# Optimization experiments

Hardware: AMD Instinct MI355X
Metric: run time of the kernel (lower is better)

The kernel has to match this reference:

```python
import jax, jax.numpy as jnp
import numpy as np

N_HEAD = 16
MASK_NEG = 1e10  # matches torch's -10000000000.0 * (1 - b)


def setup_inputs() -> dict:
    key = jax.random.key(0)
    ks = jax.random.split(key, 9)
    B, S, D = 2, 2048, 2048
    std = 0.02
    inp = {
        "x": jax.random.normal(ks[0], (B, S, D), dtype=jnp.float32),
        "Wq": jax.random.normal(ks[1], (D, D), dtype=jnp.float32) * std,
        "bq": jnp.zeros((D,), dtype=jnp.float32),
        "Wk": jax.random.normal(ks[2], (D, D), dtype=jnp.float32) * std,
        "bk": jnp.zeros((D,), dtype=jnp.float32),
        "Wv": jax.random.normal(ks[3], (D, D), dtype=jnp.float32) * std,
        "bv": jnp.zeros((D,), dtype=jnp.float32),
        "Wd": jax.random.normal(ks[4], (D, D), dtype=jnp.float32) * std,
        "bd": jnp.zeros((D,), dtype=jnp.float32),
    }
    return inp


def reference(x, Wq, bq, Wk, bk, Wv, bv, Wd, bd):
    # x: [B, S, D]; layer_past=None, query=None path (full causal prefill)
    B, S, D = x.shape
    H = N_HEAD
    hd = D // H

    def split(h):  # [B,S,D] -> [B,H,S,hd]
        return h.reshape(B, S, H, hd).transpose(0, 2, 1, 3)

    q = split(x @ Wq + bq)
    k = split(x @ Wk + bk)
    v = split(x @ Wv + bv)

    # scores [B,H,S,S]; scale=True divides by sqrt(head_dim)
    w = jnp.einsum("bhqd,bhkd->bhqk", q, k) / jnp.sqrt(jnp.float32(hd))
    b = jnp.tril(jnp.ones((S, S), dtype=w.dtype))  # causal bias buffer slice
    w = w * b - MASK_NEG * (1.0 - b)
    w = jax.nn.softmax(w, axis=-1)
    a = jnp.einsum("bhqk,bhkd->bhqd", w, v)

    a = a.transpose(0, 2, 1, 3).reshape(B, S, D)  # merge_heads
    a = a @ Wd + bd
    present = jnp.stack((k, v))  # [2, B, H, S, hd]
    return a, present
```

## Files before the change

kernel.cpp:

```cpp
#include <hip/hip_runtime.h>


typedef unsigned short ushort_t;
typedef __attribute__((ext_vector_type(8))) short short8;
typedef __attribute__((ext_vector_type(4))) float f32x4;

#define MFMA16x16x32 __builtin_amdgcn_mfma_f32_16x16x32_bf16
#define S_LEN   2048
#define DMODEL  2048
#define A_ELEMS 8388608
#define W_ELEMS 4194304

__device__ __forceinline__ ushort_t f2bf(float x) {
  unsigned u = __float_as_uint(x);
  u += 0x7FFFu + ((u >> 16) & 1u);
  return (ushort_t)(u >> 16);
}
__device__ __forceinline__ unsigned pack2(float lo, float hi) {
  return (unsigned)f2bf(lo) | ((unsigned)f2bf(hi) << 16);
}
struct f8 { float v[8]; };
__device__ __forceinline__ f8 ld8f(const float* p) {
  f8 r;
  float4 a = *(const float4*)p, b = *(const float4*)(p + 4);
  r.v[0]=a.x; r.v[1]=a.y; r.v[2]=a.z; r.v[3]=a.w;
  r.v[4]=b.x; r.v[5]=b.y; r.v[6]=b.z; r.v[7]=b.w;
  return r;
}
__device__ __forceinline__ uint4 cvt8(const f8& f) {
  uint4 o;
  o.x = pack2(f.v[0], f.v[1]); o.y = pack2(f.v[2], f.v[3]);
  o.z = pack2(f.v[4], f.v[5]); o.w = pack2(f.v[6], f.v[7]);
  return o;
}

typedef const __attribute__((address_space(1))) void* gas_t;
typedef __attribute__((address_space(3))) void* las_t;
__device__ __forceinline__ void gld16(const void* g, void* l) {
  __builtin_amdgcn_global_load_lds((gas_t)(unsigned long long)g,
                                   (las_t)(unsigned)(unsigned long long)l,
                                   16, 0, 0);
}

__global__ void __launch_bounds__(256) conv_x(const float* __restrict__ x,
                                              ushort_t* __restrict__ xb) {
  const int i = (blockIdx.x * 256 + threadIdx.x) * 8;
  f8 v = ld8f(x + i);
  *(uint4*)&xb[i] = cvt8(v);
}

__global__ void __launch_bounds__(256) trans_w(
    const float* __restrict__ w0, const float* __restrict__ w1,
    const float* __restrict__ w2, const float* __restrict__ w3,
    ushort_t* __restrict__ o0, ushort_t* __restrict__ o1,
    ushort_t* __restrict__ o2, ushort_t* __restrict__ o3) {
  __shared__ float t[64][65];
  const float* src; ushort_t* dst;
  switch (blockIdx.z) {
    case 0: src = w0; dst = o0; break;
    case 1: src = w1; dst = o1; break;
    case 2: src = w2; dst = o2; break;
    default: src = w3; dst = o3; break;
  }
  const int kb = blockIdx.y * 64, nb = blockIdx.x * 64;
  const int r = threadIdx.x >> 3, c8 = (threadIdx.x & 7) * 8;
#pragma unroll
  for (int i = 0; i < 64; i += 32) {
    *(float4*)&t[r + i][c8]     = *(const float4*)&src[(size_t)(kb + r + i) * DMODEL + nb + c8];
    *(float4*)&t[r + i][c8 + 4] = *(const float4*)&src[(size_t)(kb + r + i) * DMODEL + nb + c8 + 4];
  }
  __syncthreads();
#pragma unroll
  for (int i = 0; i < 64; i += 32) {
    float tmp[8];
#pragma unroll
    for (int j = 0; j < 8; ++j) tmp[j] = t[c8 + j][r + i];
    uint4 o;
    o.x = pack2(tmp[0], tmp[1]); o.y = pack2(tmp[2], tmp[3]);
    o.z = pack2(tmp[4], tmp[5]); o.w = pack2(tmp[6], tmp[7]);
    *(uint4*)&dst[(size_t)(nb + r + i) * DMODEL + kb + c8] = o;
  }
}

__global__ void __launch_bounds__(256) trans_v(const float* __restrict__ v,
                                               ushort_t* __restrict__ vt) {
  __shared__ float t[64][65];
  const int bh = blockIdx.z;
  const int sb = blockIdx.x * 64, db = blockIdx.y * 64;
  const float* src = v + (size_t)bh * S_LEN * 128;
  ushort_t* dst = vt + (size_t)bh * 128 * S_LEN;
  const int r = threadIdx.x >> 3, c8 = (threadIdx.x & 7) * 8;
#pragma unroll
  for (int i = 0; i < 64; i += 32) {
    *(float4*)&t[r + i][c8]     = *(const float4*)&src[(size_t)(sb + r + i) * 128 + db + c8];
    *(float4*)&t[r + i][c8 + 4] = *(const float4*)&src[(size_t)(sb + r + i) * 128 + db + c8 + 4];
  }
  __syncthreads();
#pragma unroll
  for (int i = 0; i < 64; i += 32) {
    float tmp[8];
#pragma unroll
    for (int j = 0; j < 8; ++j) tmp[j] = t[c8 + j][r + i];
    uint4 o;
    o.x = pack2(tmp[0], tmp[1]); o.y = pack2(tmp[2], tmp[3]);
    o.z = pack2(tmp[4], tmp[5]); o.w = pack2(tmp[6], tmp[7]);
    *(uint4*)&dst[(size_t)(db + r + i) * S_LEN + sb + c8] = o;
  }
}

#define ABUF (2 * 128 * 32)
#define BBUF (2 * 256 * 32)

__device__ __forceinline__ void stage6(
    const ushort_t* __restrict__ gA, const ushort_t* __restrict__ gB,
    ushort_t* An, ushort_t* Bn, int t, int w, size_t soff) {
  const size_t kc = (size_t)t * 64;
#pragma unroll
  for (int i = 0; i < 2; ++i) {
    const int c = 2 * w + i, kh = c >> 3, rg = c & 7;
    gld16(gA + (size_t)(rg * 16) * 2048 + kc + kh * 32 + soff,
          An + (kh * 128 + rg * 16) * 32);
  }
#pragma unroll
  for (int i = 0; i < 4; ++i) {
    const int c = 4 * w + i, kh = c >> 4, rg = c & 15;
    gld16(gB + (size_t)(rg * 16) * 2048 + kc + kh * 32 + soff,
          Bn + (kh * 256 + rg * 16) * 32);
  }
}

__device__ __forceinline__ void gemm2p_core(
    const ushort_t* __restrict__ gA, const ushort_t* __restrict__ gB,
    ushort_t* AsF, ushort_t* BsF, int w, int lane, f32x4 acc[4][4]) {
  const int l15 = lane & 15, quad = lane >> 4;
  const int wm = w >> 2, wn = w & 3;
  const size_t soff = (size_t)(lane >> 2) * 2048 +
                      (((lane & 3) ^ ((lane >> 3) & 3)) * 8);
  const int rslot8 = (quad ^ ((l15 >> 1) & 3)) * 8;
  const int arow = wm * 64 + l15;
  const int brow = wn * 64 + l15;

  stage6(gA, gB, AsF, BsF, 0, w, soff);
  __syncthreads();

  for (int t = 0; t < 32; ++t) {
    ushort_t* Ab = AsF + (t & 1) * ABUF;
    ushort_t* Bb = BsF + (t & 1) * BBUF;
    if (t + 1 < 32)
      stage6(gA, gB, AsF + ((t + 1) & 1) * ABUF, BsF + ((t + 1) & 1) * BBUF,
             t + 1, w, soff);
#pragma unroll
    for (int kh = 0; kh < 2; ++kh) {
      short8 af[4], bf[4];
#pragma unroll
      for (int mi = 0; mi < 4; ++mi)
        af[mi] = *(const short8*)&Ab[(kh * 128 + arow + mi * 16) * 32 + rslot8];
#pragma unroll
      for (int ni = 0; ni < 4; ++ni)
        bf[ni] = *(const short8*)&Bb[(kh * 256 + brow + ni * 16) * 32 + rslot8];
      __builtin_amdgcn_s_setprio(1);
#pragma unroll
      for (int mi = 0; mi < 4; ++mi)
#pragma unroll
        for (int ni = 0; ni < 4; ++ni)
          acc[mi][ni] = MFMA16x16x32(af[mi], bf[ni], acc[mi][ni], 0, 0, 0);
      __builtin_amdgcn_s_setprio(0);
    }
    __syncthreads();
  }
}

__global__ void __launch_bounds__(512, 2) gemm_qkv(
    const ushort_t* __restrict__ xb,
    const ushort_t* __restrict__ wtq, const ushort_t* __restrict__ wtk,
    const ushort_t* __restrict__ wtv,
    const float* __restrict__ bq, const float* __restrict__ bk,
    const float* __restrict__ bv,
    ushort_t* __restrict__ qout, float* __restrict__ kout,
    float* __restrict__ vout, ushort_t* __restrict__ kb16) {
  __shared__ ushort_t As_[2 * ABUF];
  __shared__ ushort_t Bs_[2 * BBUF];
  const int tid = threadIdx.x, w = tid >> 6, lane = tid & 63;
  const int l15 = lane & 15, quad = lane >> 4;
  const int wm = w >> 2, wn = w & 3;
  const int bx = blockIdx.x;
  const int logical = (bx & 7) * 96 + (bx >> 3);
  const int wid = logical >> 8, idx = logical & 255;
  const int tn = idx & 7, tm = idx >> 3;
  const ushort_t* Wt = wid == 0 ? wtq : (wid == 1 ? wtk : wtv);
  const float* bias = wid == 0 ? bq : (wid == 1 ? bk : bv);

  f32x4 acc[4][4] = {};
  gemm2p_core(xb + (size_t)(tm * 128) * 2048, Wt + (size_t)(tn * 256) * 2048,
              As_, Bs_, w, lane, acc);

  const int row0 = tm * 128 + wm * 64, col0 = tn * 256 + wn * 64;
#pragma unroll
  for (int ni = 0; ni < 4; ++ni) {
    const int col = col0 + ni * 16 + l15;
    const float bv_ = bias[col];
    const int h = col >> 7, d = col & 127;
#pragma unroll
    for (int mi = 0; mi < 4; ++mi) {
#pragma unroll
      for (int j = 0; j < 4; ++j) {
        const int row = row0 + mi * 16 + quad * 4 + j;
        const int b = row >> 11, s = row & 2047;
        const size_t idxg = (size_t)(((b * 16 + h) * 2048 + s)) * 128 + d;
        const float v = acc[mi][ni][j] + bv_;
        if (wid == 0) qout[idxg] = f2bf(v);
        else if (wid == 1) { kout[idxg] = v; kb16[idxg] = f2bf(v); }
        else vout[idxg] = v;
      }
    }
  }
}

__global__ void __launch_bounds__(512, 2) gemm_proj(
    const ushort_t* __restrict__ A, const ushort_t* __restrict__ Wt,
    const float* __restrict__ bias, float* __restrict__ C) {
  __shared__ ushort_t As_[2 * ABUF];
  __shared__ ushort_t Bs_[2 * BBUF];
  const int tid = threadIdx.x, w = tid >> 6, lane = tid & 63;
  const int l15 = lane & 15, quad = lane >> 4;
  const int wm = w >> 2, wn = w & 3;
  const int logical = (blockIdx.x & 7) * 32 + (blockIdx.x >> 3);
  const int tn = logical & 7, tm = logical >> 3;

  f32x4 acc[4][4] = {};
  gemm2p_core(A + (size_t)(tm * 128) * 2048, Wt + (size_t)(tn * 256) * 2048,
              As_, Bs_, w, lane, acc);

  const int row0 = tm * 128 + wm * 64, col0 = tn * 256 + wn * 64;
#pragma unroll
  for (int ni = 0; ni < 4; ++ni) {
    const int col = col0 + ni * 16 + l15;
    const float bv_ = bias[col];
#pragma unroll
    for (int mi = 0; mi < 4; ++mi)
#pragma unroll
      for (int j = 0; j < 4; ++j) {
        const int row = row0 + mi * 16 + quad * 4 + j;
        C[(size_t)row * DMODEL + col] = acc[mi][ni][j] + bv_;
      }
  }
}

__global__ void __launch_bounds__(512, 2) attn_fwd(
    const ushort_t* __restrict__ Q, const ushort_t* __restrict__ Kb,
    const ushort_t* __restrict__ Vt, ushort_t* __restrict__ O) {
  __shared__ ushort_t KP[128 * 136];
  __shared__ ushort_t Vs[128 * 128];
  const int tid = threadIdx.x;
  const int w = tid >> 6, lane = tid & 63;
  const int l15 = lane & 15, quad = lane >> 4;
  const int x7 = l15 & 7;
  const int bh = blockIdx.x & 31, pr = blockIdx.x >> 5;
  const int b = bh >> 4, h = bh & 15;
  const size_t base  = (size_t)bh * (S_LEN * 128);
  const size_t vbase = (size_t)bh * (128 * S_LEN);
  const float cs = 0.08838834764831845f * 1.4426950408889634f;

  const int srow = lane >> 4;
  const int schunk = lane & 15;

  for (int seg = 0; seg < 2; ++seg) {
    const int qt = (seg == 0) ? (15 - pr) : pr;
    const int q0 = qt * 128 + w * 16;

    short8 qf[4];
#pragma unroll
    for (int ks = 0; ks < 4; ++ks)
      qf[ks] = *(const short8*)&Q[base + (size_t)(q0 + l15) * 128 + ks * 32 + quad * 8];

    f32x4 oacc[8] = {};
    float mrun[4], lrun[4];
#pragma unroll
    for (int j = 0; j < 4; ++j) { mrun[j] = -1e30f; lrun[j] = 0.f; }

    for (int kt = 0; kt <= qt; ++kt) {
      const int kb_ = kt * 128;
      __syncthreads();
#pragma unroll
      for (int i = 0; i < 4; ++i) {
        const int r = w * 16 + i * 4 + srow;
        const int c = schunk ^ (r & 7);
        gld16(Kb + base + (size_t)(kb_ + r) * 128 + c * 8,
              (void*)(KP + (w * 16 + i * 4) * 128));
        gld16(Vt + vbase + (size_t)r * S_LEN + kb_ + c * 8,
              (void*)(Vs + (w * 16 + i * 4) * 128));
      }
      __syncthreads();

      f32x4 sacc[8] = {};
#pragma unroll
      for (int ks = 0; ks < 4; ++ks) {
        const int sw = ((ks * 4 + quad) ^ x7) * 8;
        short8 kf[8];
#pragma unroll
        for (int ni = 0; ni < 8; ++ni)
          kf[ni] = *(const short8*)&KP[(ni * 16 + l15) * 128 + sw];
#pragma unroll
        for (int ni = 0; ni < 8; ++ni)
          sacc[ni] = MFMA16x16x32(qf[ks], kf[ni], sacc[ni], 0, 0, 0);
      }
      __syncthreads();

      const bool diag = (kt == qt);
#pragma unroll
      for (int j = 0; j < 4; ++j) {
        const int rl = quad * 4 + j;
        const int rowg = q0 + rl;
        float t0[8];
        if (diag) {
#pragma unroll
          for (int ni = 0; ni < 8; ++ni) {
            const int kg = kb_ + ni * 16 + l15;
            const float s = sacc[ni][j] * cs;
            t0[ni] = (kg <= rowg) ? s : -1e30f;
          }
        } else {
#pragma unroll
          for (int ni = 0; ni < 8; ++ni) t0[ni] = sacc[ni][j] * cs;
        }
        float rm = fmaxf(fmaxf(fmaxf(t0[0], t0[1]), fmaxf(t0[2], t0[3])),
                         fmaxf(fmaxf(t0[4], t0[5]), fmaxf(t0[6], t0[7])));
        rm = fmaxf(rm, __shfl_xor(rm, 1));
        rm = fmaxf(rm, __shfl_xor(rm, 2));
        rm = fmaxf(rm, __shfl_xor(rm, 4));
        rm = fmaxf(rm, __shfl_xor(rm, 8));
        if (!__all(rm <= mrun[j] + 8.0f)) {
          const float mold = mrun[j];
          const float mnew = fmaxf(mold, rm);
          const float alpha = __builtin_amdgcn_exp2f(mold - mnew);
          lrun[j] *= alpha;
          mrun[j] = mnew;
#pragma unroll
          for (int oi = 0; oi < 8; ++oi) oacc[oi][j] *= alpha;
        }
        const float mref = mrun[j];
        float rs = 0.f;
#pragma unroll
        for (int ni = 0; ni < 8; ++ni) {
          const float pe = __builtin_amdgcn_exp2f(t0[ni] - mref);
          rs += pe;
          KP[(w * 16 + rl) * 136 + ni * 16 + l15] = f2bf(pe);
        }
        rs += __shfl_xor(rs, 1);
        rs += __shfl_xor(rs, 2);
        rs += __shfl_xor(rs, 4);
        rs += __shfl_xor(rs, 8);
        lrun[j] += rs;
      }

#pragma unroll
      for (int ks = 0; ks < 4; ++ks) {
        const int sw = ((ks * 4 + quad) ^ x7) * 8;
        short8 pf = *(const short8*)&KP[(w * 16 + l15) * 136 + ks * 32 + quad * 8];
        short8 vf[8];
#pragma unroll
        for (int oi = 0; oi < 8; ++oi)
          vf[oi] = *(const short8*)&Vs[(oi * 16 + l15) * 128 + sw];
#pragma unroll
        for (int oi = 0; oi < 8; ++oi)
          oacc[oi] = MFMA16x16x32(pf, vf[oi], oacc[oi], 0, 0, 0);
      }
    }

    {
      float inv[4];
#pragma unroll
      for (int j = 0; j < 4; ++j) inv[j] = 1.f / lrun[j];
#pragma unroll
      for (int oi = 0; oi < 8; ++oi) {
        const int oc = oi * 16 + l15;
#pragma unroll
        for (int j = 0; j < 4; ++j) {
          const int s = q0 + quad * 4 + j;
          O[((size_t)(b * S_LEN + s)) * DMODEL + h * 128 + oc] =
              f2bf(oacc[oi][j] * inv[j]);
        }
      }
    }
  }
}

extern "C" void kernel_launch(void* const* d_in, const int* in_sizes, int n_in,
                              void* d_out, int out_size, void* d_ws,
                              size_t ws_size, hipStream_t stream) {
  const float* x  = (const float*)d_in[0];
  const float* Wq = (const float*)d_in[1];
  const float* bq = (const float*)d_in[2];
  const float* Wk = (const float*)d_in[3];
  const float* bk = (const float*)d_in[4];
  const float* Wv = (const float*)d_in[5];
  const float* bv = (const float*)d_in[6];
  const float* Wd = (const float*)d_in[7];
  const float* bd = (const float*)d_in[8];

  float* out   = (float*)d_out;
  float* a_out = out;
  float* k_out = out + A_ELEMS;
  float* v_out = out + 2 * A_ELEMS;
  ushort_t* ob  = (ushort_t*)d_out;
  ushort_t* xb   = ob;
  ushort_t* q_ws = ob + A_ELEMS;

  ushort_t* ws  = (ushort_t*)d_ws;
  ushort_t* wtq = ws;
  ushort_t* wtk = ws + W_ELEMS;
  ushort_t* wtv = ws + 2 * (size_t)W_ELEMS;
  ushort_t* wtd = ws + 3 * (size_t)W_ELEMS;
  ushort_t* attn_ws = ws + 4 * (size_t)W_ELEMS;
  ushort_t* kb_ws   = attn_ws + (size_t)A_ELEMS;
  ushort_t* vt_ws   = attn_ws + 2 * (size_t)A_ELEMS;

  conv_x<<<4096, 256, 0, stream>>>(x, xb);
  trans_w<<<dim3(32, 32, 4), 256, 0, stream>>>(Wq, Wk, Wv, Wd,
                                               wtq, wtk, wtv, wtd);
  gemm_qkv<<<768, 512, 0, stream>>>(xb, wtq, wtk, wtv, bq, bk, bv,
                                    q_ws, k_out, v_out, kb_ws);
  trans_v<<<dim3(32, 2, 32), 256, 0, stream>>>(v_out, vt_ws);
  attn_fwd<<<256, 512, 0, stream>>>(q_ws, kb_ws, vt_ws, attn_ws);
  gemm_proj<<<256, 512, 0, stream>>>(attn_ws, wtd, bd, a_out);
}
```

Baseline: 446.6 us.

## Fuse V transpose into QKV GEMM epilogue and split attention blocks by rows

The separate trans_v kernel is removed. Instead, the V-producing blocks of the QKV GEMM stage their bf16 tile in shared memory and write the transposed V directly, which avoids re-reading the fp32 V and one kernel launch. The attention kernel now runs 512 blocks of 256 threads, each handling 64 query rows instead of 128. This raises block count and occupancy, but each block loads the same K/V tiles, so K/V loads are doubled.

```diff
diff --git a/kernel.cpp b/kernel.cpp
--- a/kernel.cpp
+++ b/kernel.cpp
@@ -82,32 +82,6 @@
   }
 }
 
-__global__ void __launch_bounds__(256) trans_v(const float* __restrict__ v,
-                                               ushort_t* __restrict__ vt) {
-  __shared__ float t[64][65];
-  const int bh = blockIdx.z;
-  const int sb = blockIdx.x * 64, db = blockIdx.y * 64;
-  const float* src = v + (size_t)bh * S_LEN * 128;
-  ushort_t* dst = vt + (size_t)bh * 128 * S_LEN;
-  const int r = threadIdx.x >> 3, c8 = (threadIdx.x & 7) * 8;
-#pragma unroll
-  for (int i = 0; i < 64; i += 32) {
-    *(float4*)&t[r + i][c8]     = *(const float4*)&src[(size_t)(sb + r + i) * 128 + db + c8];
-    *(float4*)&t[r + i][c8 + 4] = *(const float4*)&src[(size_t)(sb + r + i) * 128 + db + c8 + 4];
-  }
-  __syncthreads();
-#pragma unroll
-  for (int i = 0; i < 64; i += 32) {
-    float tmp[8];
-#pragma unroll
-    for (int j = 0; j < 8; ++j) tmp[j] = t[c8 + j][r + i];
-    uint4 o;
-    o.x = pack2(tmp[0], tmp[1]); o.y = pack2(tmp[2], tmp[3]);
-    o.z = pack2(tmp[4], tmp[5]); o.w = pack2(tmp[6], tmp[7]);
-    *(uint4*)&dst[(size_t)(db + r + i) * S_LEN + sb + c8] = o;
-  }
-}
-
 #define ABUF (2 * 128 * 32)
 #define BBUF (2 * 256 * 32)
 
@@ -177,7 +151,8 @@
     const float* __restrict__ bq, const float* __restrict__ bk,
     const float* __restrict__ bv,
     ushort_t* __restrict__ qout, float* __restrict__ kout,
-    float* __restrict__ vout, ushort_t* __restrict__ kb16) {
+    float* __restrict__ vout, ushort_t* __restrict__ kb16,
+    ushort_t* __restrict__ vt16) {
   __shared__ ushort_t As_[2 * ABUF];
   __shared__ ushort_t Bs_[2 * BBUF];
   const int tid = threadIdx.x, w = tid >> 6, lane = tid & 63;
@@ -214,6 +189,38 @@
       }
     }
   }
+
+  if (wid == 2) {
+    ushort_t* T = Bs_;
+    const int s0 = (tm & 15) * 128;
+    const int bh0 = (tm >> 4) * 16 + tn * 2;
+    for (int hh = 0; hh < 2; ++hh) {
+      __syncthreads();
+      if ((wn >> 1) == hh) {
+#pragma unroll
+        for (int ni = 0; ni < 4; ++ni) {
+          const int cl = (wn & 1) * 64 + ni * 16 + l15;
+          const float bv_ = bias[col0 + ni * 16 + l15];
+#pragma unroll
+          for (int mi = 0; mi < 4; ++mi) {
+            const int r4 = wm * 64 + mi * 16 + quad * 4;
+            uint2 p;
+            p.x = pack2(acc[mi][ni][0] + bv_, acc[mi][ni][1] + bv_);
+            p.y = pack2(acc[mi][ni][2] + bv_, acc[mi][ni][3] + bv_);
+            *(uint2*)&T[cl * 136 + r4] = p;
+          }
+        }
+      }
+      __syncthreads();
+#pragma unroll
+      for (int ii = 0; ii < 4; ++ii) {
+        const int ch = ii * 512 + tid;
+        const int d = ch >> 4, sc = ch & 15;
+        const uint4 v4 = *(const uint4*)&T[d * 136 + sc * 8];
+        *(uint4*)&vt16[((size_t)((bh0 + hh) * 128 + d)) * 2048 + s0 + sc * 8] = v4;
+      }
+    }
+  }
 }
 
 __global__ void __launch_bounds__(512, 2) gemm_proj(
@@ -246,7 +253,7 @@
   }
 }
 
-__global__ void __launch_bounds__(512, 2) attn_fwd(
+__global__ void __launch_bounds__(256, 2) attn_fwd(
     const ushort_t* __restrict__ Q, const ushort_t* __restrict__ Kb,
     const ushort_t* __restrict__ Vt, ushort_t* __restrict__ O) {
   __shared__ ushort_t KP[128 * 136];
@@ -255,7 +262,8 @@
   const int w = tid >> 6, lane = tid & 63;
   const int l15 = lane & 15, quad = lane >> 4;
   const int x7 = l15 & 7;
-  const int bh = blockIdx.x & 31, pr = blockIdx.x >> 5;
+  const int bh = blockIdx.x & 31, pq = blockIdx.x >> 5;
+  const int pr = pq & 7, rh = pq >> 3;
   const int b = bh >> 4, h = bh & 15;
   const size_t base  = (size_t)bh * (S_LEN * 128);
   const size_t vbase = (size_t)bh * (128 * S_LEN);
@@ -266,7 +274,7 @@
 
   for (int seg = 0; seg < 2; ++seg) {
     const int qt = (seg == 0) ? (15 - pr) : pr;
-    const int q0 = qt * 128 + w * 16;
+    const int q0 = qt * 128 + rh * 64 + w * 16;
 
     short8 qf[4];
 #pragma unroll
@@ -282,13 +290,13 @@
       const int kb_ = kt * 128;
       __syncthreads();
 #pragma unroll
-      for (int i = 0; i < 4; ++i) {
-        const int r = w * 16 + i * 4 + srow;
+      for (int i = 0; i < 8; ++i) {
+        const int r = w * 32 + i * 4 + srow;
         const int c = schunk ^ (r & 7);
         gld16(Kb + base + (size_t)(kb_ + r) * 128 + c * 8,
-              (void*)(KP + (w * 16 + i * 4) * 128));
+              (void*)(KP + (w * 32 + i * 4) * 128));
         gld16(Vt + vbase + (size_t)r * S_LEN + kb_ + c * 8,
-              (void*)(Vs + (w * 16 + i * 4) * 128));
+              (void*)(Vs + (w * 32 + i * 4) * 128));
       }
       __syncthreads();
 
@@ -419,8 +427,7 @@
   trans_w<<<dim3(32, 32, 4), 256, 0, stream>>>(Wq, Wk, Wv, Wd,
                                                wtq, wtk, wtv, wtd);
   gemm_qkv<<<768, 512, 0, stream>>>(xb, wtq, wtk, wtv, bq, bk, bv,
-                                    q_ws, k_out, v_out, kb_ws);
-  trans_v<<<dim3(32, 2, 32), 256, 0, stream>>>(v_out, vt_ws);
-  attn_fwd<<<256, 512, 0, stream>>>(q_ws, kb_ws, vt_ws, attn_ws);
+                                    q_ws, k_out, v_out, kb_ws, vt_ws);
+  attn_fwd<<<512, 256, 0, stream>>>(q_ws, kb_ws, vt_ws, attn_ws);
   gemm_proj<<<256, 512, 0, stream>>>(attn_ws, wtd, bd, a_out);
 }
```

Measured after the change: 440.1 us. Within noise of the previous version (-1.5%).
